# Optimization experiments

Measured on AMD Instinct MI355X. Metric: run time of the kernel, lower is better.

The kernel has to match this reference:

```python
import jax, jax.numpy as jnp
import numpy as np

E = 32  # embed_dim
B = 524288


def _mha(q_tok, kv_tok, Wi, bi, Wo, bo):
    """Single-head torch-style MultiheadAttention (batch_first).
    Wi: [3E, E] packed q/k/v in_proj; Wo: [E, E] out_proj.
    q_tok: [B, Lq, E], kv_tok: [B, Lk, E].
    """
    Wq, Wk, Wv = Wi[:E], Wi[E:2 * E], Wi[2 * E:]
    bq, bk, bv = bi[:E], bi[E:2 * E], bi[2 * E:]
    q = q_tok @ Wq.T + bq
    k = kv_tok @ Wk.T + bk
    v = kv_tok @ Wv.T + bv
    scores = jnp.einsum('bqd,bkd->bqk', q, k) / jnp.sqrt(jnp.asarray(E, q.dtype))
    attn = jax.nn.softmax(scores, axis=-1)
    out = jnp.einsum('bqk,bkd->bqd', attn, v)
    return out @ Wo.T + bo


def setup_inputs() -> dict:
    key = jax.random.key(0)
    ks = jax.random.split(key, 14)
    s = 0.1
    return {
        'groupA_feats': jax.random.normal(ks[0], (B, 3), jnp.float32),
        'groupB_feats': jax.random.normal(ks[1], (B, 2), jnp.float32),
        'WA': jax.random.normal(ks[2], (E, 1), jnp.float32) * s,
        'bA': jax.random.normal(ks[3], (E,), jnp.float32) * s,
        'WB': jax.random.normal(ks[4], (E, 1), jnp.float32) * s,
        'bB': jax.random.normal(ks[5], (E,), jnp.float32) * s,
        'Wi_AB': jax.random.normal(ks[6], (3 * E, E), jnp.float32) * s,
        'bi_AB': jax.random.normal(ks[7], (3 * E,), jnp.float32) * s,
        'Wo_AB': jax.random.normal(ks[8], (E, E), jnp.float32) * s,
        'bo_AB': jnp.zeros((E,), jnp.float32),
        'Wi_BA': jax.random.normal(ks[9], (3 * E, E), jnp.float32) * s,
        'bi_BA': jax.random.normal(ks[10], (3 * E,), jnp.float32) * s,
        'Wo_BA': jax.random.normal(ks[11], (E, E), jnp.float32) * s,
        'bo_BA': jnp.zeros((E,), jnp.float32),
        'Wf': jax.random.normal(ks[12], (1, E), jnp.float32) * s,
        'bf': jax.random.normal(ks[13], (1,), jnp.float32) * s,
    }


def reference(groupA_feats, groupB_feats, WA, bA, WB, bB,
              Wi_AB, bi_AB, Wo_AB, bo_AB, Wi_BA, bi_BA, Wo_BA, bo_BA,
              Wf, bf):
    # Per-feature Linear(1, E) embeddings, vectorized over the feature dim:
    # A_tokens[b, i, :] = groupA[b, i] * WA[:, 0] + bA
    A_tokens = groupA_feats[:, :, None] * WA[:, 0][None, None, :] + bA  # [B,3,E]
    B_tokens = groupB_feats[:, :, None] * WB[:, 0][None, None, :] + bB  # [B,2,E]
    crossAB = _mha(A_tokens, B_tokens, Wi_AB, bi_AB, Wo_AB, bo_AB)      # [B,3,E]
    crossBA = _mha(B_tokens, A_tokens, Wi_BA, bi_BA, Wo_BA, bo_BA)      # [B,2,E]
    combined = (crossAB.mean(axis=1) + crossBA.mean(axis=1)) * 0.5       # [B,E]
    out = combined @ Wf.T + bf                                           # [B,1]
    return jnp.where(out >= 0, out, 0.01 * out)  # LeakyReLU(0.01)
```

## Files before the change

### kernel.cpp

```cpp
#include <hip/hip_runtime.h>
#include <math.h>


__global__ void precompute_consts(
    const float* __restrict__ WA, const float* __restrict__ bA,
    const float* __restrict__ WB, const float* __restrict__ bB,
    const float* __restrict__ WiAB, const float* __restrict__ biAB,
    const float* __restrict__ WoAB, const float* __restrict__ boAB,
    const float* __restrict__ WiBA, const float* __restrict__ biBA,
    const float* __restrict__ WoBA, const float* __restrict__ boBA,
    const float* __restrict__ Wf, const float* __restrict__ bf,
    float* __restrict__ consts)
{
    __shared__ float uq[2][32], uk[2][32], cq[2][32], uv[2][32], cv[2][32];
    __shared__ float p[2][32], r[2][32];
    const int e = threadIdx.x;
    if (e < 32) {
        float s_uq = 0.f, s_uk = 0.f, s_cq = 0.f, s_uv = 0.f, s_cv = 0.f;
        for (int d = 0; d < 32; ++d) {
            const float wq = WiAB[e * 32 + d];
            const float wk = WiAB[(32 + e) * 32 + d];
            const float wv = WiAB[(64 + e) * 32 + d];
            s_uq += wq * WA[d];
            s_cq += wq * bA[d];
            s_uk += wk * WB[d];
            s_uv += wv * WB[d];
            s_cv += wv * bB[d];
        }
        uq[0][e] = s_uq; uk[0][e] = s_uk; cq[0][e] = s_cq + biAB[e];
        uv[0][e] = s_uv; cv[0][e] = s_cv + biAB[64 + e];

        s_uq = 0.f; s_uk = 0.f; s_cq = 0.f; s_uv = 0.f; s_cv = 0.f;
        for (int d = 0; d < 32; ++d) {
            const float wq = WiBA[e * 32 + d];
            const float wk = WiBA[(32 + e) * 32 + d];
            const float wv = WiBA[(64 + e) * 32 + d];
            s_uq += wq * WB[d];
            s_cq += wq * bB[d];
            s_uk += wk * WA[d];
            s_uv += wv * WA[d];
            s_cv += wv * bA[d];
        }
        uq[1][e] = s_uq; uk[1][e] = s_uk; cq[1][e] = s_cq + biBA[e];
        uv[1][e] = s_uv; cv[1][e] = s_cv + biBA[64 + e];
    }
    __syncthreads();
    if (e < 32) {
        float pAB = 0.f, rAB = 0.f, pBA = 0.f, rBA = 0.f;
        for (int d = 0; d < 32; ++d) {
            pAB += WoAB[e * 32 + d] * uv[0][d];
            rAB += WoAB[e * 32 + d] * cv[0][d];
            pBA += WoBA[e * 32 + d] * uv[1][d];
            rBA += WoBA[e * 32 + d] * cv[1][d];
        }
        p[0][e] = pAB; r[0][e] = rAB + boAB[e];
        p[1][e] = pBA; r[1][e] = rBA + boBA[e];
    }
    __syncthreads();
    if (e == 0) {
        float aAB = 0.f, gAB = 0.f, aBA = 0.f, gBA = 0.f;
        float c1 = 0.f, c2 = 0.f, c0 = 0.f;
        for (int d = 0; d < 32; ++d) {
            aAB += uq[0][d] * uk[0][d];
            gAB += cq[0][d] * uk[0][d];
            aBA += uq[1][d] * uk[1][d];
            gBA += cq[1][d] * uk[1][d];
            c1  += Wf[d] * p[0][d];
            c2  += Wf[d] * p[1][d];
            c0  += Wf[d] * (r[0][d] + r[1][d]);
        }
        const float inv_sqrt_e = 0.17677669529663688f;
        consts[0] = aAB * inv_sqrt_e;
        consts[1] = gAB * inv_sqrt_e;
        consts[2] = aBA * inv_sqrt_e;
        consts[3] = gBA * inv_sqrt_e;
        consts[4] = 0.5f * c0 + bf[0];
        consts[5] = 0.5f * c1;
        consts[6] = 0.5f * c2;
    }
}

__device__ __forceinline__ float sigmoidf_(float x) {
    return 1.0f / (1.0f + expf(-x));
}

__global__ void fused_main(const float* __restrict__ Af,
                           const float* __restrict__ Bf,
                           const float* __restrict__ consts,
                           float* __restrict__ out, int n)
{
    const float kaAB = consts[0], kgAB = consts[1];
    const float kaBA = consts[2], kgBA = consts[3];
    const float c0 = consts[4], c1 = consts[5], c2 = consts[6];

    const int i = blockIdx.x * blockDim.x + threadIdx.x;
    if (i >= n) return;

    const float a0 = Af[3 * i + 0];
    const float a1 = Af[3 * i + 1];
    const float a2 = Af[3 * i + 2];
    const float2 bb = *reinterpret_cast<const float2*>(Bf + 2 * i);
    const float b0 = bb.x, b1 = bb.y;

    const float dB = b0 - b1;
    const float s0 = b1 + dB * sigmoidf_(dB * (kaAB * a0 + kgAB));
    const float s1 = b1 + dB * sigmoidf_(dB * (kaAB * a1 + kgAB));
    const float s2 = b1 + dB * sigmoidf_(dB * (kaAB * a2 + kgAB));
    const float S_AB = (s0 + s1 + s2) * (1.0f / 3.0f);

    float S_BA = 0.f;
    #pragma unroll
    for (int j = 0; j < 2; ++j) {
        const float bj = (j == 0) ? b0 : b1;
        const float c = kaBA * bj + kgBA;
        const float l0 = a0 * c, l1 = a1 * c, l2 = a2 * c;
        const float m = fmaxf(l0, fmaxf(l1, l2));
        const float e0 = expf(l0 - m), e1 = expf(l1 - m), e2 = expf(l2 - m);
        S_BA += (e0 * a0 + e1 * a1 + e2 * a2) / (e0 + e1 + e2);
    }
    S_BA *= 0.5f;

    const float y = c0 + c1 * S_AB + c2 * S_BA;
    out[i] = (y >= 0.f) ? y : 0.01f * y;
}

extern "C" void kernel_launch(void* const* d_in, const int* in_sizes, int n_in,
                              void* d_out, int out_size, void* d_ws, size_t ws_size,
                              hipStream_t stream) {
    const float* groupA = (const float*)d_in[0];
    const float* groupB = (const float*)d_in[1];
    const float* WA   = (const float*)d_in[2];
    const float* bA   = (const float*)d_in[3];
    const float* WB   = (const float*)d_in[4];
    const float* bB   = (const float*)d_in[5];
    const float* WiAB = (const float*)d_in[6];
    const float* biAB = (const float*)d_in[7];
    const float* WoAB = (const float*)d_in[8];
    const float* boAB = (const float*)d_in[9];
    const float* WiBA = (const float*)d_in[10];
    const float* biBA = (const float*)d_in[11];
    const float* WoBA = (const float*)d_in[12];
    const float* boBA = (const float*)d_in[13];
    const float* Wf   = (const float*)d_in[14];
    const float* bf   = (const float*)d_in[15];

    float* out = (float*)d_out;
    float* consts = (float*)d_ws;

    const int n = in_sizes[0] / 3;

    precompute_consts<<<1, 64, 0, stream>>>(
        WA, bA, WB, bB, WiAB, biAB, WoAB, boAB,
        WiBA, biBA, WoBA, boBA, Wf, bf, consts);

    const int block = 256;
    const int grid = (n + block - 1) / block;
    fused_main<<<grid, block, 0, stream>>>(groupA, groupB, consts, out, n);
}
```

Measured before the change: 95.31 us.

## Fuse constant precompute into main kernel with grid-stride loop

Removes the separate single-block precompute launch by having every block recompute the folded attention constants in shared memory before processing elements. The main kernel becomes a grid-stride loop over a fixed 1024-block grid, with float4-vectorized weight dot products. This removes one launch and the serial dependency between the kernels, but every block now redundantly reads the weights and runs a serial 32-step reduction on one thread before its elementwise work starts.

```diff
diff --git a/kernel.cpp b/kernel.cpp
--- a/kernel.cpp
+++ b/kernel.cpp
@@ -2,7 +2,17 @@
 #include <math.h>
 
 
-__global__ void precompute_consts(
+__device__ __forceinline__ float dot4(float4 a, float4 b) {
+    return a.x * b.x + a.y * b.y + a.z * b.z + a.w * b.w;
+}
+
+__device__ __forceinline__ float sigmoidf_(float x) {
+    return 1.0f / (1.0f + expf(-x));
+}
+
+__global__ __launch_bounds__(256) void fused_all(
+    const float* __restrict__ Af,
+    const float* __restrict__ Bf,
     const float* __restrict__ WA, const float* __restrict__ bA,
     const float* __restrict__ WB, const float* __restrict__ bB,
     const float* __restrict__ WiAB, const float* __restrict__ biAB,
@@ -10,118 +20,118 @@
     const float* __restrict__ WiBA, const float* __restrict__ biBA,
     const float* __restrict__ WoBA, const float* __restrict__ boBA,
     const float* __restrict__ Wf, const float* __restrict__ bf,
-    float* __restrict__ consts)
+    float* __restrict__ out, int n)
 {
     __shared__ float uq[2][32], uk[2][32], cq[2][32], uv[2][32], cv[2][32];
-    __shared__ float p[2][32], r[2][32];
-    const int e = threadIdx.x;
-    if (e < 32) {
-        float s_uq = 0.f, s_uk = 0.f, s_cq = 0.f, s_uv = 0.f, s_cv = 0.f;
-        for (int d = 0; d < 32; ++d) {
-            const float wq = WiAB[e * 32 + d];
-            const float wk = WiAB[(32 + e) * 32 + d];
-            const float wv = WiAB[(64 + e) * 32 + d];
-            s_uq += wq * WA[d];
-            s_cq += wq * bA[d];
-            s_uk += wk * WB[d];
-            s_uv += wv * WB[d];
-            s_cv += wv * bB[d];
+    __shared__ float pp[2][32], rr[2][32];
+    __shared__ float cst[7];
+    const int t = threadIdx.x;
+
+    if (t < 64) {
+        const int side = t >> 5;
+        const int e = t & 31;
+        const float* Wi  = side ? WiBA : WiAB;
+        const float* bi  = side ? biBA : biAB;
+        const float* wqv = side ? WB : WA;
+        const float* bqv = side ? bB : bA;
+        const float* wkv = side ? WA : WB;
+        const float* bkv = side ? bA : bB;
+
+        const float4* rq = (const float4*)(Wi + e * 32);
+        const float4* rk = (const float4*)(Wi + (32 + e) * 32);
+        const float4* rv = (const float4*)(Wi + (64 + e) * 32);
+        const float4* q4 = (const float4*)wqv;
+        const float4* qb = (const float4*)bqv;
+        const float4* k4 = (const float4*)wkv;
+        const float4* kb = (const float4*)bkv;
+
+        float s_uq = 0.f, s_cq = 0.f, s_uk = 0.f, s_uv = 0.f, s_cv = 0.f;
+        #pragma unroll
+        for (int d = 0; d < 8; ++d) {
+            const float4 wq = rq[d], wk = rk[d], wv = rv[d];
+            s_uq += dot4(wq, q4[d]);
+            s_cq += dot4(wq, qb[d]);
+            s_uk += dot4(wk, k4[d]);
+            s_uv += dot4(wv, k4[d]);
+            s_cv += dot4(wv, kb[d]);
         }
-        uq[0][e] = s_uq; uk[0][e] = s_uk; cq[0][e] = s_cq + biAB[e];
-        uv[0][e] = s_uv; cv[0][e] = s_cv + biAB[64 + e];
-
-        s_uq = 0.f; s_uk = 0.f; s_cq = 0.f; s_uv = 0.f; s_cv = 0.f;
-        for (int d = 0; d < 32; ++d) {
-            const float wq = WiBA[e * 32 + d];
-            const float wk = WiBA[(32 + e) * 32 + d];
-            const float wv = WiBA[(64 + e) * 32 + d];
-            s_uq += wq * WB[d];
-            s_cq += wq * bB[d];
-            s_uk += wk * WA[d];
-            s_uv += wv * WA[d];
-            s_cv += wv * bA[d];
-        }
-        uq[1][e] = s_uq; uk[1][e] = s_uk; cq[1][e] = s_cq + biBA[e];
-        uv[1][e] = s_uv; cv[1][e] = s_cv + biBA[64 + e];
+        uq[side][e] = s_uq; cq[side][e] = s_cq + bi[e];
+        uk[side][e] = s_uk; uv[side][e] = s_uv; cv[side][e] = s_cv + bi[64 + e];
     }
     __syncthreads();
-    if (e < 32) {
-        float pAB = 0.f, rAB = 0.f, pBA = 0.f, rBA = 0.f;
-        for (int d = 0; d < 32; ++d) {
-            pAB += WoAB[e * 32 + d] * uv[0][d];
-            rAB += WoAB[e * 32 + d] * cv[0][d];
-            pBA += WoBA[e * 32 + d] * uv[1][d];
-            rBA += WoBA[e * 32 + d] * cv[1][d];
+    if (t < 64) {
+        const int side = t >> 5;
+        const int e = t & 31;
+        const float* Wo = side ? WoBA : WoAB;
+        const float* bo = side ? boBA : boAB;
+        const float4* ro = (const float4*)(Wo + e * 32);
+        const float4* v4 = (const float4*)uv[side];
+        const float4* c4 = (const float4*)cv[side];
+        float sp = 0.f, sr = 0.f;
+        #pragma unroll
+        for (int d = 0; d < 8; ++d) {
+            const float4 w = ro[d];
+            sp += dot4(w, v4[d]);
+            sr += dot4(w, c4[d]);
         }
-        p[0][e] = pAB; r[0][e] = rAB + boAB[e];
-        p[1][e] = pBA; r[1][e] = rBA + boBA[e];
+        pp[side][e] = sp; rr[side][e] = sr + bo[e];
     }
     __syncthreads();
-    if (e == 0) {
+    if (t == 0) {
         float aAB = 0.f, gAB = 0.f, aBA = 0.f, gBA = 0.f;
-        float c1 = 0.f, c2 = 0.f, c0 = 0.f;
+        float c0 = 0.f, c1 = 0.f, c2 = 0.f;
+        #pragma unroll
         for (int d = 0; d < 32; ++d) {
             aAB += uq[0][d] * uk[0][d];
             gAB += cq[0][d] * uk[0][d];
             aBA += uq[1][d] * uk[1][d];
             gBA += cq[1][d] * uk[1][d];
-            c1  += Wf[d] * p[0][d];
-            c2  += Wf[d] * p[1][d];
-            c0  += Wf[d] * (r[0][d] + r[1][d]);
+            c1  += Wf[d] * pp[0][d];
+            c2  += Wf[d] * pp[1][d];
+            c0  += Wf[d] * (rr[0][d] + rr[1][d]);
         }
-        const float inv_sqrt_e = 0.17677669529663688f;
-        consts[0] = aAB * inv_sqrt_e;
-        consts[1] = gAB * inv_sqrt_e;
-        consts[2] = aBA * inv_sqrt_e;
-        consts[3] = gBA * inv_sqrt_e;
-        consts[4] = 0.5f * c0 + bf[0];
-        consts[5] = 0.5f * c1;
-        consts[6] = 0.5f * c2;
+        const float is = 0.17677669529663688f;
+        cst[0] = aAB * is; cst[1] = gAB * is;
+        cst[2] = aBA * is; cst[3] = gBA * is;
+        cst[4] = 0.5f * c0 + bf[0];
+        cst[5] = 0.5f * c1;
+        cst[6] = 0.5f * c2;
     }
-}
+    __syncthreads();
 
-__device__ __forceinline__ float sigmoidf_(float x) {
-    return 1.0f / (1.0f + expf(-x));
-}
+    const float kaAB = cst[0], kgAB = cst[1];
+    const float kaBA = cst[2], kgBA = cst[3];
+    const float c0 = cst[4], c1 = cst[5], c2 = cst[6];
 
-__global__ void fused_main(const float* __restrict__ Af,
-                           const float* __restrict__ Bf,
-                           const float* __restrict__ consts,
-                           float* __restrict__ out, int n)
-{
-    const float kaAB = consts[0], kgAB = consts[1];
-    const float kaBA = consts[2], kgBA = consts[3];
-    const float c0 = consts[4], c1 = consts[5], c2 = consts[6];
+    const int stride = gridDim.x * blockDim.x;
+    for (int i = blockIdx.x * blockDim.x + t; i < n; i += stride) {
+        const float a0 = Af[3 * i + 0];
+        const float a1 = Af[3 * i + 1];
+        const float a2 = Af[3 * i + 2];
+        const float2 bb = *reinterpret_cast<const float2*>(Bf + 2 * i);
+        const float b0 = bb.x, b1 = bb.y;
 
-    const int i = blockIdx.x * blockDim.x + threadIdx.x;
-    if (i >= n) return;
+        const float dB = b0 - b1;
+        const float s0 = b1 + dB * sigmoidf_(dB * (kaAB * a0 + kgAB));
+        const float s1 = b1 + dB * sigmoidf_(dB * (kaAB * a1 + kgAB));
+        const float s2 = b1 + dB * sigmoidf_(dB * (kaAB * a2 + kgAB));
+        const float S_AB = (s0 + s1 + s2) * (1.0f / 3.0f);
 
-    const float a0 = Af[3 * i + 0];
-    const float a1 = Af[3 * i + 1];
-    const float a2 = Af[3 * i + 2];
-    const float2 bb = *reinterpret_cast<const float2*>(Bf + 2 * i);
-    const float b0 = bb.x, b1 = bb.y;
+        float S_BA = 0.f;
+        #pragma unroll
+        for (int j = 0; j < 2; ++j) {
+            const float bj = (j == 0) ? b0 : b1;
+            const float c = kaBA * bj + kgBA;
+            const float l0 = a0 * c, l1 = a1 * c, l2 = a2 * c;
+            const float m = fmaxf(l0, fmaxf(l1, l2));
+            const float e0 = expf(l0 - m), e1 = expf(l1 - m), e2 = expf(l2 - m);
+            S_BA += (e0 * a0 + e1 * a1 + e2 * a2) / (e0 + e1 + e2);
+        }
+        S_BA *= 0.5f;
 
-    const float dB = b0 - b1;
-    const float s0 = b1 + dB * sigmoidf_(dB * (kaAB * a0 + kgAB));
-    const float s1 = b1 + dB * sigmoidf_(dB * (kaAB * a1 + kgAB));
-    const float s2 = b1 + dB * sigmoidf_(dB * (kaAB * a2 + kgAB));
-    const float S_AB = (s0 + s1 + s2) * (1.0f / 3.0f);
-
-    float S_BA = 0.f;
-    #pragma unroll
-    for (int j = 0; j < 2; ++j) {
-        const float bj = (j == 0) ? b0 : b1;
-        const float c = kaBA * bj + kgBA;
-        const float l0 = a0 * c, l1 = a1 * c, l2 = a2 * c;
-        const float m = fmaxf(l0, fmaxf(l1, l2));
-        const float e0 = expf(l0 - m), e1 = expf(l1 - m), e2 = expf(l2 - m);
-        S_BA += (e0 * a0 + e1 * a1 + e2 * a2) / (e0 + e1 + e2);
+        const float y = c0 + c1 * S_AB + c2 * S_BA;
+        out[i] = (y >= 0.f) ? y : 0.01f * y;
     }
-    S_BA *= 0.5f;
-
-    const float y = c0 + c1 * S_AB + c2 * S_BA;
-    out[i] = (y >= 0.f) ? y : 0.01f * y;
 }
 
 extern "C" void kernel_launch(void* const* d_in, const int* in_sizes, int n_in,
@@ -145,15 +155,12 @@
     const float* bf   = (const float*)d_in[15];
 
     float* out = (float*)d_out;
-    float* consts = (float*)d_ws;
-
     const int n = in_sizes[0] / 3;
 
-    precompute_consts<<<1, 64, 0, stream>>>(
-        WA, bA, WB, bB, WiAB, biAB, WoAB, boAB,
-        WiBA, biBA, WoBA, boBA, Wf, bf, consts);
-
     const int block = 256;
-    const int grid = (n + block - 1) / block;
-    fused_main<<<grid, block, 0, stream>>>(groupA, groupB, consts, out, n);
+    const int grid = 1024;
+    fused_all<<<grid, block, 0, stream>>>(
+        groupA, groupB, WA, bA, WB, bB,
+        WiAB, biAB, WoAB, boAB, WiBA, biBA, WoBA, boBA,
+        Wf, bf, out, n);
 }
```

New measurement: 96.62 us. Within noise of the previous version (+1.4%).
